# Performance work log

Hardware: AMD Instinct MI355X
Metric: run time of the kernel (lower is better)

The kernel has to match this reference:

```python
import jax, jax.numpy as jnp
import numpy as np
import math

C_IN, L, D, H, DFF = 16, 1024, 128, 8, 512
B = 16
EPS = 1e-5


def layer_norm(x, g, b):
    mu = jnp.mean(x, axis=-1, keepdims=True)
    var = jnp.var(x, axis=-1, keepdims=True)
    return (x - mu) * jax.lax.rsqrt(var + EPS) * g + b


def tape_pe():
    pos = jnp.arange(L, dtype=jnp.float32)[:, None]
    div = jnp.exp(jnp.arange(0, D, 2, dtype=jnp.float32) * (-math.log(10000.0) / D))
    ang = pos * div * (D / L)  # [L, D/2]
    return jnp.stack([jnp.sin(ang), jnp.cos(ang)], axis=-1).reshape(L, D)


def setup_inputs() -> dict:
    key = jax.random.key(0)
    ks = jax.random.split(key, 16)
    d4 = 4 * D
    inp = {
        "x": jax.random.normal(ks[0], (B, C_IN, L), dtype=jnp.float32),
        "conv1_w": jax.random.normal(ks[1], (d4, 1, 1, 7), dtype=jnp.float32) * 0.2,
        "conv1_b": jnp.zeros((d4,), jnp.float32),
        "bn1_g": jnp.ones((d4,), jnp.float32),
        "bn1_b": jnp.zeros((d4,), jnp.float32),
        "conv2_w": jax.random.normal(ks[2], (D, d4, C_IN, 1), dtype=jnp.float32) * (1.0 / math.sqrt(d4 * C_IN)),
        "conv2_b": jnp.zeros((D,), jnp.float32),
        "bn2_g": jnp.ones((D,), jnp.float32),
        "bn2_b": jnp.zeros((D,), jnp.float32),
        "wq": jax.random.normal(ks[3], (D, D), dtype=jnp.float32) / math.sqrt(D),
        "wk": jax.random.normal(ks[4], (D, D), dtype=jnp.float32) / math.sqrt(D),
        "wv": jax.random.normal(ks[5], (D, D), dtype=jnp.float32) / math.sqrt(D),
        "rel_table": jax.random.normal(ks[6], (2 * L - 1, H), dtype=jnp.float32) * 0.02,
        "ln_att_g": jnp.ones((D,), jnp.float32),
        "ln_att_b": jnp.zeros((D,), jnp.float32),
        "ln1_g": jnp.ones((D,), jnp.float32),
        "ln1_b": jnp.zeros((D,), jnp.float32),
        "ln2_g": jnp.ones((D,), jnp.float32),
        "ln2_b": jnp.zeros((D,), jnp.float32),
        "ff_w1": jax.random.normal(ks[7], (DFF, D), dtype=jnp.float32) / math.sqrt(D),
        "ff_b1": jnp.zeros((DFF,), jnp.float32),
        "ff_w2": jax.random.normal(ks[8], (D, DFF), dtype=jnp.float32) / math.sqrt(DFF),
        "ff_b2": jnp.zeros((D,), jnp.float32),
    }
    return inp


def reference(x, conv1_w, conv1_b, bn1_g, bn1_b, conv2_w, conv2_b, bn2_g, bn2_b,
              wq, wk, wv, rel_table, ln_att_g, ln_att_b, ln1_g, ln1_b,
              ln2_g, ln2_b, ff_w1, ff_b1, ff_w2, ff_b2):
    dn = ("NCHW", "OIHW", "NCHW")
    h = x[:, None, :, :]  # [B,1,C_IN,L]
    h = jax.lax.conv_general_dilated(h, conv1_w, (1, 1), ((0, 0), (3, 3)), dimension_numbers=dn)
    h = h + conv1_b[None, :, None, None]
    # BatchNorm2d in eval with running_mean=0, running_var=1
    h = h * (bn1_g * (1.0 / math.sqrt(1.0 + EPS)))[None, :, None, None] + bn1_b[None, :, None, None]
    h = jax.nn.gelu(h, approximate=False)
    h = jax.lax.conv_general_dilated(h, conv2_w, (1, 1), ((0, 0), (0, 0)), dimension_numbers=dn)
    h = h + conv2_b[None, :, None, None]
    h = h * (bn2_g * (1.0 / math.sqrt(1.0 + EPS)))[None, :, None, None] + bn2_b[None, :, None, None]
    h = jax.nn.gelu(h, approximate=False)
    x_src = jnp.transpose(h[:, :, 0, :], (0, 2, 1))  # [B,L,D]

    x_pos = x_src + tape_pe()  # tAPE (dropout is identity in eval)

    dh = D // H
    scale = D ** (-0.5)  # note: full d_model, as in the source
    q = (x_pos @ wq.T).reshape(B, L, H, dh).transpose(0, 2, 1, 3)
    k = (x_pos @ wk.T).reshape(B, L, H, dh).transpose(0, 2, 1, 3)
    v = (x_pos @ wv.T).reshape(B, L, H, dh).transpose(0, 2, 1, 3)
    scores = jnp.einsum("bhqd,bhkd->bhqk", q, k) * scale
    attn = jax.nn.softmax(scores, axis=-1)
    # gathered relative-position bias added AFTER softmax (faithful to source)
    idx = jnp.arange(L)[:, None] - jnp.arange(L)[None, :] + (L - 1)  # [L,L]
    rel_bias = rel_table[idx]  # [L,L,H]
    attn = attn + jnp.transpose(rel_bias, (2, 0, 1))[None]
    out = jnp.einsum("bhqk,bhkd->bhqd", attn, v).transpose(0, 2, 1, 3).reshape(B, L, D)
    out = layer_norm(out, ln_att_g, ln_att_b)  # Attention_Rel_Scl.to_out

    att = layer_norm(x_src + out, ln1_g, ln1_b)
    ff = jax.nn.relu(att @ ff_w1.T + ff_b1) @ ff_w2.T + ff_b2
    y = layer_norm(att + ff, ln2_g, ln2_b)
    return jnp.transpose(y, (0, 2, 1))  # [B,D,L]
```

## Files before the change

kernel.cpp:

```cpp
#include <hip/hip_runtime.h>
#include <math.h>

#define BB   16
#define CIN  16
#define LL   1024
#define DD   128
#define NHH  8
#define DHH  16
#define DF   512

#define INVS 0.9999950000374998f
#define QSCALE 0.08838834764831845f

typedef __attribute__((ext_vector_type(4))) float f32x4;
typedef __attribute__((ext_vector_type(8))) __bf16 bf16x8;

__device__ __forceinline__ float gelu_t(float v) {
    float u = v * v;
    float a = v * fmaf(-0.07135481627f, u, -1.5957691216f);
    float e = __expf(a);
    return v * __builtin_amdgcn_rcpf(1.0f + e);
}

__device__ __forceinline__ unsigned pkbf(float a, float b) {
    union { __bf16 h[2]; unsigned u; } z;
    z.h[0] = (__bf16)a; z.h[1] = (__bf16)b;
    return z.u;
}

#define SWZ(l) ((((l) & 7) ^ (((l) >> 2) & 6)))

__global__ __launch_bounds__(256) void k_prep(
    const float* __restrict__ c2w,
    const float* __restrict__ wq, const float* __restrict__ wk,
    const float* __restrict__ wv,
    const float* __restrict__ w1f, const float* __restrict__ w2f,
    const float* __restrict__ c1w, const float* __restrict__ c1b,
    const float* __restrict__ g1,  const float* __restrict__ bb1,
    __bf16* __restrict__ w2bf,  __bf16* __restrict__ wallbf,
    __bf16* __restrict__ w1fbf, __bf16* __restrict__ w2fbf,
    float* __restrict__ peb, float* __restrict__ w1A, float* __restrict__ b1A)
{
    const int bid = blockIdx.x;
    const int t = threadIdx.x;
    if (bid < 1024) {
        int i = (bid * 256 + t) * 4;
        float4 v = *(const float4*)&c2w[i];
        union { __bf16 h[4]; float2 f2; } u;
        u.h[0] = (__bf16)v.x; u.h[1] = (__bf16)v.y;
        u.h[2] = (__bf16)v.z; u.h[3] = (__bf16)v.w;
        *(float2*)&w2bf[i] = u.f2;
    } else if (bid < 1072) {
        int e = ((bid - 1024) * 256 + t) * 4;
        int sel = e >> 14, r = e & 16383;
        const float* src = (sel == 0) ? wq : ((sel == 1) ? wk : wv);
        float sc = (sel == 0) ? QSCALE : 1.0f;
        float4 v = *(const float4*)&src[r];
        union { __bf16 h[4]; float2 f2; } u;
        u.h[0] = (__bf16)(v.x * sc); u.h[1] = (__bf16)(v.y * sc);
        u.h[2] = (__bf16)(v.z * sc); u.h[3] = (__bf16)(v.w * sc);
        *(float2*)&wallbf[e] = u.f2;
    } else if (bid < 1136) {
        int e = ((bid - 1072) * 256 + t) * 4;
        float4 v = *(const float4*)&w1f[e];
        union { __bf16 h[4]; float2 f2; } u;
        u.h[0] = (__bf16)v.x; u.h[1] = (__bf16)v.y;
        u.h[2] = (__bf16)v.z; u.h[3] = (__bf16)v.w;
        *(float2*)&w1fbf[e] = u.f2;
    } else if (bid < 1200) {
        int e = ((bid - 1136) * 256 + t) * 4;
        float4 v = *(const float4*)&w2f[e];
        union { __bf16 h[4]; float2 f2; } u;
        u.h[0] = (__bf16)v.x; u.h[1] = (__bf16)v.y;
        u.h[2] = (__bf16)v.z; u.h[3] = (__bf16)v.w;
        *(float2*)&w2fbf[e] = u.f2;
    } else if (bid < 1456) {
        int p = (bid - 1200) * 256 + t;
        int l = p >> 6, jj = p & 63;
        float ang = (float)l * expf(-0.14391156831212787f * (float)jj) * 0.125f;
        peb[l * 128 + jj * 2]     = sinf(ang);
        peb[l * 128 + jj * 2 + 1] = cosf(ang);
    } else {
        for (int o = t; o < DF; o += 256) {
            float A = g1[o] * INVS;
            #pragma unroll
            for (int tp = 0; tp < 7; tp++) w1A[o * 8 + tp] = c1w[o * 7 + tp] * A;
            w1A[o * 8 + 7] = 0.0f;
            b1A[o] = fmaf(c1b[o], A, bb1[o]);
        }
    }
}

__global__ __launch_bounds__(256) void k_conv(
    const float* __restrict__ x,
    const float* __restrict__ w1A, const float* __restrict__ b1A,
    const __bf16* __restrict__ w2bf,
    const float* __restrict__ c2b, const float* __restrict__ g2,
    const float* __restrict__ bb2,
    float* __restrict__ xsrc)
{
    const int lt = blockIdx.x;
    const int b  = blockIdx.y;
    const int t  = threadIdx.x;
    const int l0 = lt * 32;

    __shared__ float xs[CIN][40];
    __shared__ __align__(16) __bf16 Ab[2][32 * 128];

    for (int idx = t; idx < CIN * 38; idx += 256) {
        int c = idx / 38, i = idx % 38;
        int l = l0 - 3 + i;
        xs[c][i] = (l >= 0 && l < LL) ? x[(b * CIN + c) * LL + l] : 0.0f;
    }
    __syncthreads();

    const int cp  = t & 7;
    const int lqi = (t >> 3) & 7;
    const int ogu = __builtin_amdgcn_readfirstlane(t >> 6);
    const int c0  = cp * 2;
    const int lq  = lqi * 4;

    float xw[2][10];
    #pragma unroll
    for (int j = 0; j < 10; j++) {
        xw[0][j] = xs[c0][lq + j];
        xw[1][j] = xs[c0 + 1][lq + j];
    }

    const int lane = t & 63;
    const int l15 = lane & 15, kg = lane >> 4;
    const int nw = t >> 6;

    f32x4 acc[2][2];
    #pragma unroll
    for (int mf = 0; mf < 2; mf++)
        #pragma unroll
        for (int nf = 0; nf < 2; nf++) acc[mf][nf] = (f32x4){0.f, 0.f, 0.f, 0.f};

    bf16x8 breg[2][8];

#define BLOAD(CH, BUF) do { \
    _Pragma("unroll") \
    for (int nf = 0; nf < 2; nf++) \
        _Pragma("unroll") \
        for (int kk = 0; kk < 4; kk++) \
            breg[BUF][nf * 4 + kk] = *(const bf16x8*)&w2bf[ \
                (size_t)(nw * 32 + nf * 16 + l15) * 8192 + (size_t)(CH) * 128 + kk * 32 + kg * 8]; \
} while (0)

#define CONV_CHUNK(BUF, CH) do { \
    _Pragma("unroll") \
    for (int j = 0; j < 2; j++) { \
        int o = (CH) * 8 + ogu * 2 + j; \
        f32x4 wA = *(const f32x4*)&w1A[o * 8]; \
        f32x4 wB = *(const f32x4*)&w1A[o * 8 + 4]; \
        float bias = b1A[o]; \
        int kcol = (ogu * 2 + j) * 16 + c0; \
        _Pragma("unroll") \
        for (int dl = 0; dl < 4; dl++) { \
            float h2[2]; \
            _Pragma("unroll") \
            for (int ci = 0; ci < 2; ci++) { \
                float s = fmaf(xw[ci][dl], wA[0], bias); \
                s = fmaf(xw[ci][dl + 1], wA[1], s); \
                s = fmaf(xw[ci][dl + 2], wA[2], s); \
                s = fmaf(xw[ci][dl + 3], wA[3], s); \
                s = fmaf(xw[ci][dl + 4], wB[0], s); \
                s = fmaf(xw[ci][dl + 5], wB[1], s); \
                s = fmaf(xw[ci][dl + 6], wB[2], s); \
                h2[ci] = gelu_t(s); \
            } \
            int l = lq + dl; \
            *(unsigned*)&Ab[BUF][l * 128 + (kcol ^ (SWZ(l) << 3))] = pkbf(h2[0], h2[1]); \
        } \
    } \
} while (0)

#define MFMA_CHUNK(BUF, BI) do { \
    _Pragma("unroll") \
    for (int kk = 0; kk < 4; kk++) { \
        int kb = kk * 32 + kg * 8; \
        bf16x8 af[2]; \
        _Pragma("unroll") \
        for (int mf = 0; mf < 2; mf++) { \
            int r = mf * 16 + l15; \
            af[mf] = *(const bf16x8*)&Ab[BUF][r * 128 + (kb ^ (SWZ(r) << 3))]; \
        } \
        _Pragma("unroll") \
        for (int mf = 0; mf < 2; mf++) \
            _Pragma("unroll") \
            for (int nf = 0; nf < 2; nf++) \
                acc[mf][nf] = __builtin_amdgcn_mfma_f32_16x16x32_bf16( \
                    af[mf], breg[BI][nf * 4 + kk], acc[mf][nf], 0, 0, 0); \
    } \
} while (0)

    BLOAD(0, 0);
    CONV_CHUNK(0, 0);
    __syncthreads();

    for (int ic = 0; ic < 62; ic += 2) {
        BLOAD(ic + 1, 1);
        MFMA_CHUNK(0, 0);
        CONV_CHUNK(1, ic + 1);
        __syncthreads();

        BLOAD(ic + 2, 0);
        MFMA_CHUNK(1, 1);
        CONV_CHUNK(0, ic + 2);
        __syncthreads();
    }
    BLOAD(63, 1);
    MFMA_CHUNK(0, 0);
    CONV_CHUNK(1, 63);
    __syncthreads();
    MFMA_CHUNK(1, 1);

    #pragma unroll
    for (int mf = 0; mf < 2; mf++) {
        #pragma unroll
        for (int nf = 0; nf < 2; nf++) {
            int d = nw * 32 + nf * 16 + l15;
            float A2 = g2[d] * INVS;
            float B2 = fmaf(c2b[d], A2, bb2[d]);
            #pragma unroll
            for (int r = 0; r < 4; r++) {
                int l = l0 + mf * 16 + kg * 4 + r;
                xsrc[((size_t)b * LL + l) * DD + d] = gelu_t(fmaf(acc[mf][nf][r], A2, B2));
            }
        }
    }
#undef BLOAD
#undef CONV_CHUNK
#undef MFMA_CHUNK
}

__global__ __launch_bounds__(384) void k_qkv(
    const float* __restrict__ xsrc, const float* __restrict__ peb,
    const __bf16* __restrict__ wallbf,
    __bf16* __restrict__ qo, __bf16* __restrict__ ko, __bf16* __restrict__ vo)
{
    const int lt = blockIdx.x, b = blockIdx.y;
    const int t = threadIdx.x;
    const int l0 = lt * 64;

    __shared__ __align__(16) __bf16 Xp[64 * 128];

    for (int e = t; e < 2048; e += 384) {
        int l = e >> 5, d0 = (e & 31) * 4;
        float4 xv = *(const float4*)&xsrc[((size_t)b * LL + l0 + l) * DD + d0];
        float4 pv = *(const float4*)&peb[(size_t)(l0 + l) * DD + d0];
        union { __bf16 h[4]; float2 f2; } u;
        u.h[0] = (__bf16)(xv.x + pv.x); u.h[1] = (__bf16)(xv.y + pv.y);
        u.h[2] = (__bf16)(xv.z + pv.z); u.h[3] = (__bf16)(xv.w + pv.w);
        *(float2*)&Xp[l * 128 + (d0 ^ (SWZ(l) << 3))] = u.f2;
    }
    __syncthreads();

    const int w = t >> 6, lane = t & 63;
    const int l15 = lane & 15, kg = lane >> 4;
    const int wsel = w >> 1, hb = w & 1;

    bf16x8 breg[16];
    #pragma unroll
    for (int nf = 0; nf < 4; nf++)
        #pragma unroll
        for (int kk = 0; kk < 4; kk++)
            breg[nf * 4 + kk] = *(const bf16x8*)&wallbf[
                (size_t)wsel * 16384 + (size_t)(hb * 64 + nf * 16 + l15) * 128 + kk * 32 + kg * 8];

    f32x4 acc[4][4];
    #pragma unroll
    for (int mf = 0; mf < 4; mf++)
        #pragma unroll
        for (int nf = 0; nf < 4; nf++) acc[mf][nf] = (f32x4){0.f, 0.f, 0.f, 0.f};

    #pragma unroll
    for (int kk = 0; kk < 4; kk++) {
        int kb = kk * 32 + kg * 8;
        bf16x8 af[4];
        #pragma unroll
        for (int mf = 0; mf < 4; mf++) {
            int r = mf * 16 + l15;
            af[mf] = *(const bf16x8*)&Xp[r * 128 + (kb ^ (SWZ(r) << 3))];
        }
        #pragma unroll
        for (int mf = 0; mf < 4; mf++)
            #pragma unroll
            for (int nf = 0; nf < 4; nf++)
                acc[mf][nf] = __builtin_amdgcn_mfma_f32_16x16x32_bf16(
                    af[mf], breg[nf * 4 + kk], acc[mf][nf], 0, 0, 0);
    }

    __bf16* op = (wsel == 0) ? qo : ((wsel == 1) ? ko : vo);
    #pragma unroll
    for (int mf = 0; mf < 4; mf++) {
        #pragma unroll
        for (int nf = 0; nf < 4; nf++) {
            int h = hb * 4 + nf;
            #pragma unroll
            for (int r = 0; r < 4; r++) {
                int l = l0 + mf * 16 + kg * 4 + r;
                op[(((size_t)b * NHH + h) * LL + l) * DHH + l15] = (__bf16)acc[mf][nf][r];
            }
        }
    }
}

__global__ __launch_bounds__(256) void k_attn(
    const __bf16* __restrict__ q, const __bf16* __restrict__ k,
    const __bf16* __restrict__ v, const float* __restrict__ rel,
    float* __restrict__ out)
{
    const int bh = blockIdx.x;
    const int qt = blockIdx.y;
    const int h  = bh & 7;
    const int t  = threadIdx.x;
    const int w  = t >> 6, lane = t & 63;
    const int g  = lane >> 4, qi = lane & 15;
    const int xq = (qi & 7) << 3;
    const int qbase = qt * 128 + w * 32;

    __shared__ __align__(16) __bf16 lds[16384];
    __bf16* Vl = lds;
    __bf16* Pw = lds + 4096 + w * 2048;
    __bf16* R0 = lds + 12288;
    __bf16* R1 = lds + 14336;

    for (int i = t; i < 2048; i += 256) {
        R0[i] = (__bf16)((i <= 2046) ? rel[(size_t)(2046 - i) * NHH + h] : 0.0f);
        R1[i] = (__bf16)((i <= 2045) ? rel[(size_t)(2045 - i) * NHH + h] : 0.0f);
    }

    bf16x8 qf[2];
    {
        union { unsigned u[4]; bf16x8 v8; } uz;
        uz.u[0] = uz.u[1] = uz.u[2] = uz.u[3] = 0u;
        #pragma unroll
        for (int n = 0; n < 2; n++) {
            qf[n] = uz.v8;
            if (g < 2)
                qf[n] = *(const bf16x8*)&q[((size_t)bh * LL + qbase + n * 16 + qi) * DHH + g * 8];
        }
    }

    f32x4 accp[2], accb[2];
    #pragma unroll
    for (int n = 0; n < 2; n++) {
        accp[n] = (f32x4){0.f, 0.f, 0.f, 0.f};
        accb[n] = (f32x4){0.f, 0.f, 0.f, 0.f};
    }
    float mrun[2] = {-INFINITY, -INFINITY};
    float lrun[2] = {0.f, 0.f};

    const f32x4 zero4 = (f32x4){0.f, 0.f, 0.f, 0.f};

#define PROC_N(Sn, n) do { \
    float mx = Sn[0][0]; \
    _Pragma("unroll") \
    for (int f = 0; f < 8; f++) { \
        _Pragma("unroll") \
        for (int r = 0; r < 4; r++) if (f || r) mx = fmaxf(mx, Sn[f][r]); } \
    mx = fmaxf(mx, __shfl_xor(mx, 16, 64)); \
    mx = fmaxf(mx, __shfl_xor(mx, 32, 64)); \
    float mnew = fmaxf(mrun[n], mx); \
    float sf = __expf(mrun[n] - mnew); \
    mrun[n] = mnew; \
    lrun[n] *= sf; \
    accp[n][0] *= sf; accp[n][1] *= sf; accp[n][2] *= sf; accp[n][3] *= sf; \
    float ls = 0.f; \
    _Pragma("unroll") \
    for (int f = 0; f < 8; f++) { \
        float p0 = __expf(Sn[f][0] - mnew), p1 = __expf(Sn[f][1] - mnew); \
        float p2 = __expf(Sn[f][2] - mnew), p3 = __expf(Sn[f][3] - mnew); \
        ls += (p0 + p1) + (p2 + p3); \
        unsigned* pp = (unsigned*)(Pw + (qi * 128 + ((f * 16 + g * 4) ^ xq))); \
        pp[0] = pkbf(p0, p1); pp[1] = pkbf(p2, p3); \
    } \
    ls += __shfl_xor(ls, 16, 64); ls += __shfl_xor(ls, 32, 64); \
    lrun[n] += ls; \
    int qoff = 1023 - (qbase + (n) * 16 + qi) + k0; \
    _Pragma("unroll") \
    for (int c = 0; c < 4; c++) { \
        bf16x8 vf = *(const bf16x8*)&Vbuf[qi * 128 + ((c * 32 + g * 8) ^ xq)]; \
        bf16x8 pf = *(const bf16x8*)&Pw[qi * 128 + ((c * 32 + g * 8) ^ xq)]; \
        int idx = qoff + c * 32 + 8 * g; \
        const unsigned* tb = (const unsigned*)((idx & 1) ? R1 : R0); \
        unsigned s_ = (unsigned)idx >> 1; \
        union { unsigned u[4]; bf16x8 v8; } bu; \
        bu.u[0] = tb[s_]; bu.u[1] = tb[s_ + 1]; \
        bu.u[2] = tb[s_ + 2]; bu.u[3] = tb[s_ + 3]; \
        accp[n] = __builtin_amdgcn_mfma_f32_16x16x32_bf16(vf, pf, accp[n], 0, 0, 0); \
        accb[n] = __builtin_amdgcn_mfma_f32_16x16x32_bf16(vf, bu.v8, accb[n], 0, 0, 0); \
    } \
} while (0)

    for (int kt = 0; kt < 8; kt++) {
        const int k0 = kt * 128;
        {
            int kr = t >> 1, d0 = (t & 1) * 8;
            bf16x8 b8 = *(const bf16x8*)&v[((size_t)bh * LL + k0 + kr) * DHH + d0];
            __bf16* dst = Vl + (kt & 1) * 2048;
            #pragma unroll
            for (int i = 0; i < 8; i++) {
                int d = d0 + i;
                dst[d * 128 + (kr ^ ((d & 7) << 3))] = b8[i];
            }
        }
        __syncthreads();
        const __bf16* Vbuf = Vl + (kt & 1) * 2048;

        f32x4 S0[8], S1[8];
        #pragma unroll
        for (int f = 0; f < 8; f++) {
            bf16x8 kf = *(const bf16x8*)&k[((size_t)bh * LL + k0 + f * 16 + qi) * DHH + (g & 1) * 8];
            S0[f] = __builtin_amdgcn_mfma_f32_16x16x32_bf16(kf, qf[0], zero4, 0, 0, 0);
            S1[f] = __builtin_amdgcn_mfma_f32_16x16x32_bf16(kf, qf[1], zero4, 0, 0, 0);
        }

        PROC_N(S0, 0);
        PROC_N(S1, 1);
    }
#undef PROC_N

    #pragma unroll
    for (int n = 0; n < 2; n++) {
        float inv = 1.0f / lrun[n];
        float4 o;
        o.x = accp[n][0] * inv + accb[n][0];
        o.y = accp[n][1] * inv + accb[n][1];
        o.z = accp[n][2] * inv + accb[n][2];
        o.w = accp[n][3] * inv + accb[n][3];
        *(float4*)&out[((size_t)bh * LL + qbase + n * 16 + qi) * DHH + g * 4] = o;
    }
}

__global__ __launch_bounds__(256) void k_ln(
    const float* __restrict__ ao,  const float* __restrict__ xsrc,
    const float* __restrict__ lag, const float* __restrict__ lab,
    const float* __restrict__ l1g, const float* __restrict__ l1b,
    float* __restrict__ att)
{
    const int lt = blockIdx.x, b = blockIdx.y;
    const int t = threadIdx.x;
    const int l0 = lt * 64;
    __shared__ float tile[64][132];

    #pragma unroll
    for (int u = 0; u < 4; u++) {
        int cid = u * 256 + t;
        int hh = cid >> 7, rem = cid & 127;
        int l = rem >> 1, dh0 = (rem & 1) * 8;
        const float* src = &ao[(((size_t)b * NHH + hh) * LL + l0 + l) * DHH + dh0];
        float4 a0 = *(const float4*)src;
        float4 a1 = *(const float4*)(src + 4);
        *(float4*)&tile[l][hh * 16 + dh0]     = a0;
        *(float4*)&tile[l][hh * 16 + dh0 + 4] = a1;
    }
    __syncthreads();

    const int wid = t >> 6, lane = t & 63;
    float2 ga  = *(const float2*)&lag[lane * 2];
    float2 ba  = *(const float2*)&lab[lane * 2];
    float2 g1v = *(const float2*)&l1g[lane * 2];
    float2 b1v = *(const float2*)&l1b[lane * 2];

    for (int rr = 0; rr < 16; rr++) {
        int r = wid * 16 + rr;
        float2 vv = *(const float2*)&tile[r][lane * 2];
        float s = vv.x + vv.y, s2 = vv.x * vv.x + vv.y * vv.y;
        #pragma unroll
        for (int m = 1; m < 64; m <<= 1) { s += __shfl_xor(s, m, 64); s2 += __shfl_xor(s2, m, 64); }
        float mu = s * (1.f / 128.f);
        float var = s2 * (1.f / 128.f) - mu * mu;
        float rs = rsqrtf(var + 1e-5f);
        float o0 = (vv.x - mu) * rs * ga.x + ba.x;
        float o1 = (vv.y - mu) * rs * ga.y + ba.y;
        float2 xv = *(const float2*)&xsrc[((size_t)b * LL + l0 + r) * DD + lane * 2];
        float t0 = xv.x + o0, t1 = xv.y + o1;
        s = t0 + t1; s2 = t0 * t0 + t1 * t1;
        #pragma unroll
        for (int m = 1; m < 64; m <<= 1) { s += __shfl_xor(s, m, 64); s2 += __shfl_xor(s2, m, 64); }
        mu = s * (1.f / 128.f);
        var = s2 * (1.f / 128.f) - mu * mu;
        rs = rsqrtf(var + 1e-5f);
        float a0 = (t0 - mu) * rs * g1v.x + b1v.x;
        float a1 = (t1 - mu) * rs * g1v.y + b1v.y;
        float2 o = {a0, a1};
        *(float2*)&att[((size_t)b * LL + l0 + r) * DD + lane * 2] = o;
    }
}

__global__ __launch_bounds__(512) void k_ff1(
    const float* __restrict__ att, const __bf16* __restrict__ w1fbf,
    const float* __restrict__ b1f, __bf16* __restrict__ ff1b)
{
    const int lt = blockIdx.x, b = blockIdx.y;
    const int t = threadIdx.x;
    const int l0 = lt * 64;

    __shared__ __align__(16) __bf16 Ax[64 * 128];

    #pragma unroll
    for (int it = 0; it < 4; it++) {
        int e = it * 512 + t;
        int l = e >> 5, d0 = (e & 31) * 4;
        float4 xv = *(const float4*)&att[((size_t)b * LL + l0 + l) * DD + d0];
        union { __bf16 h[4]; float2 f2; } u;
        u.h[0] = (__bf16)xv.x; u.h[1] = (__bf16)xv.y;
        u.h[2] = (__bf16)xv.z; u.h[3] = (__bf16)xv.w;
        *(float2*)&Ax[l * 128 + (d0 ^ (SWZ(l) << 3))] = u.f2;
    }
    __syncthreads();

    const int w = t >> 6, lane = t & 63;
    const int l15 = lane & 15, kg = lane >> 4;

    bf16x8 breg[16];
    #pragma unroll
    for (int nf = 0; nf < 4; nf++)
        #pragma unroll
        for (int kk = 0; kk < 4; kk++)
            breg[nf * 4 + kk] = *(const bf16x8*)&w1fbf[
                (size_t)(w * 64 + nf * 16 + l15) * 128 + kk * 32 + kg * 8];

    f32x4 acc[4][4];
    #pragma unroll
    for (int mf = 0; mf < 4; mf++)
        #pragma unroll
        for (int nf = 0; nf < 4; nf++) acc[mf][nf] = (f32x4){0.f, 0.f, 0.f, 0.f};

    #pragma unroll
    for (int kk = 0; kk < 4; kk++) {
        int kb = kk * 32 + kg * 8;
        bf16x8 af[4];
        #pragma unroll
        for (int mf = 0; mf < 4; mf++) {
            int r = mf * 16 + l15;
            af[mf] = *(const bf16x8*)&Ax[r * 128 + (kb ^ (SWZ(r) << 3))];
        }
        #pragma unroll
        for (int mf = 0; mf < 4; mf++)
            #pragma unroll
            for (int nf = 0; nf < 4; nf++)
                acc[mf][nf] = __builtin_amdgcn_mfma_f32_16x16x32_bf16(
                    af[mf], breg[nf * 4 + kk], acc[mf][nf], 0, 0, 0);
    }

    #pragma unroll
    for (int nf = 0; nf < 4; nf++) {
        int n = w * 64 + nf * 16 + l15;
        float bias = b1f[n];
        #pragma unroll
        for (int mf = 0; mf < 4; mf++) {
            #pragma unroll
            for (int r = 0; r < 4; r++) {
                int l = l0 + mf * 16 + kg * 4 + r;
                float vv = fmaxf(acc[mf][nf][r] + bias, 0.0f);
                ff1b[((size_t)b * LL + l) * DF + n] = (__bf16)vv;
            }
        }
    }
}

__global__ __launch_bounds__(512) void k_ff2(
    const __bf16* __restrict__ ff1b, const __bf16* __restrict__ w2fbf,
    const float* __restrict__ b2f, const float* __restrict__ att,
    const float* __restrict__ l2g, const float* __restrict__ l2b,
    float* __restrict__ y)
{
    const int lt = blockIdx.x, b = blockIdx.y;
    const int t = threadIdx.x;
    const int l0 = lt * 64;

    __shared__ __align__(16) __bf16 Ax[64 * 512];
    float* yl = (float*)Ax;

    #pragma unroll
    for (int it = 0; it < 8; it++) {
        int g8 = it * 512 + t;
        int l = g8 >> 6, c8 = g8 & 63;
        bf16x8 v8 = *(const bf16x8*)&ff1b[((size_t)b * LL + l0 + l) * DF + c8 * 8];
        *(bf16x8*)&Ax[l * 512 + ((c8 * 8) ^ (SWZ(l) << 3))] = v8;
    }
    __syncthreads();

    const int w = t >> 6, lane = t & 63;
    const int l15 = lane & 15, kg = lane >> 4;
    const int d = w * 16 + l15;

    bf16x8 breg[16];
    #pragma unroll
    for (int kk = 0; kk < 16; kk++)
        breg[kk] = *(const bf16x8*)&w2fbf[(size_t)d * DF + kk * 32 + kg * 8];

    f32x4 acc[4];
    #pragma unroll
    for (int mf = 0; mf < 4; mf++) acc[mf] = (f32x4){0.f, 0.f, 0.f, 0.f};

    #pragma unroll
    for (int kk = 0; kk < 16; kk++) {
        int kb = kk * 32 + kg * 8;
        #pragma unroll
        for (int mf = 0; mf < 4; mf++) {
            int r = mf * 16 + l15;
            bf16x8 af = *(const bf16x8*)&Ax[r * 512 + (kb ^ (SWZ(r) << 3))];
            acc[mf] = __builtin_amdgcn_mfma_f32_16x16x32_bf16(af, breg[kk], acc[mf], 0, 0, 0);
        }
    }
    __syncthreads();

    {
        float bias = b2f[d];
        #pragma unroll
        for (int mf = 0; mf < 4; mf++) {
            #pragma unroll
            for (int r = 0; r < 4; r++) {
                int l = mf * 16 + kg * 4 + r;
                float res = att[((size_t)b * LL + l0 + l) * DD + d];
                yl[l * 132 + d] = acc[mf][r] + bias + res;
            }
        }
    }
    __syncthreads();

    const int wid = t >> 6;
    float2 gv = *(const float2*)&l2g[lane * 2];
    float2 bv = *(const float2*)&l2b[lane * 2];
    for (int rr = 0; rr < 8; rr++) {
        int r = wid * 8 + rr;
        float2 vv = *(const float2*)&yl[r * 132 + lane * 2];
        float s = vv.x + vv.y, s2 = vv.x * vv.x + vv.y * vv.y;
        #pragma unroll
        for (int m = 1; m < 64; m <<= 1) { s += __shfl_xor(s, m, 64); s2 += __shfl_xor(s2, m, 64); }
        float mu = s * (1.f / 128.f);
        float var = s2 * (1.f / 128.f) - mu * mu;
        float rs = rsqrtf(var + 1e-5f);
        float o0 = (vv.x - mu) * rs * gv.x + bv.x;
        float o1 = (vv.y - mu) * rs * gv.y + bv.y;
        yl[r * 132 + lane * 2]     = o0;
        yl[r * 132 + lane * 2 + 1] = o1;
    }
    __syncthreads();

    {
        int dd = t >> 2, lh = (t & 3) * 16;
        #pragma unroll
        for (int i0 = 0; i0 < 16; i0 += 4) {
            float4 o = { yl[(lh + i0 + 0) * 132 + dd], yl[(lh + i0 + 1) * 132 + dd],
                         yl[(lh + i0 + 2) * 132 + dd], yl[(lh + i0 + 3) * 132 + dd] };
            *(float4*)&y[(size_t)b * DD * LL + (size_t)dd * LL + l0 + lh + i0] = o;
        }
    }
}

extern "C" void kernel_launch(void* const* d_in, const int* in_sizes, int n_in,
                              void* d_out, int out_size, void* d_ws, size_t ws_size,
                              hipStream_t stream)
{
    const float* x   = (const float*)d_in[0];
    const float* c1w = (const float*)d_in[1];
    const float* c1b = (const float*)d_in[2];
    const float* g1  = (const float*)d_in[3];
    const float* bb1 = (const float*)d_in[4];
    const float* c2w = (const float*)d_in[5];
    const float* c2b = (const float*)d_in[6];
    const float* g2  = (const float*)d_in[7];
    const float* bb2 = (const float*)d_in[8];
    const float* wq  = (const float*)d_in[9];
    const float* wk  = (const float*)d_in[10];
    const float* wv  = (const float*)d_in[11];
    const float* rel = (const float*)d_in[12];
    const float* lag = (const float*)d_in[13];
    const float* lab = (const float*)d_in[14];
    const float* l1g = (const float*)d_in[15];
    const float* l1b = (const float*)d_in[16];
    const float* l2g = (const float*)d_in[17];
    const float* l2b = (const float*)d_in[18];
    const float* w1f = (const float*)d_in[19];
    const float* b1f = (const float*)d_in[20];
    const float* w2f = (const float*)d_in[21];
    const float* b2f = (const float*)d_in[22];

    char* W = (char*)d_ws;
    const size_t MB = 1ull << 20;
    float*  xsrc   = (float*)(W);
    float*  abuf   = (float*)(W + 8 * MB);
    float*  attb   = (float*)(W + 16 * MB);
    __bf16* qbuf   = (__bf16*)(W + 24 * MB);
    __bf16* kbuf   = (__bf16*)(W + 28 * MB);
    __bf16* vbuf   = (__bf16*)(W + 32 * MB);
    __bf16* ff1b   = (__bf16*)(W + 36 * MB);
    __bf16* w2bf   = (__bf16*)(W + 52 * MB);
    __bf16* wallbf = (__bf16*)(W + 54 * MB);
    __bf16* w1fbf  = (__bf16*)(W + 54 * MB + 128 * 1024);
    __bf16* w2fbf  = (__bf16*)(W + 54 * MB + 256 * 1024);
    float*  peb    = (float*)(W + 54 * MB + 384 * 1024);
    float*  w1A    = (float*)(W + 54 * MB + 896 * 1024);
    float*  b1A    = (float*)(W + 54 * MB + 912 * 1024);

    k_prep<<<dim3(1457), dim3(256), 0, stream>>>(
        c2w, wq, wk, wv, w1f, w2f, c1w, c1b, g1, bb1,
        w2bf, wallbf, w1fbf, w2fbf, peb, w1A, b1A);
    k_conv<<<dim3(32, 16), dim3(256), 0, stream>>>(x, w1A, b1A, w2bf, c2b, g2, bb2, xsrc);
    k_qkv<<<dim3(16, 16), dim3(384), 0, stream>>>(xsrc, peb, wallbf, qbuf, kbuf, vbuf);
    k_attn<<<dim3(128, 8), dim3(256), 0, stream>>>(qbuf, kbuf, vbuf, rel, abuf);
    k_ln<<<dim3(16, 16), dim3(256), 0, stream>>>(abuf, xsrc, lag, lab, l1g, l1b, attb);
    k_ff1<<<dim3(16, 16), dim3(512), 0, stream>>>(attb, w1fbf, b1f, ff1b);
    k_ff2<<<dim3(16, 16), dim3(512), 0, stream>>>(ff1b, w2fbf, b2f, attb, l2g, l2b, (float*)d_out);
}
```

Measured before the change: 246.4 us.

## Use 512-thread conv blocks with 256-wide K chunks and one N-fragment per wave

The fused conv kernel moves from 4 to 8 waves per block. Each wave now owns one 16-column output fragment instead of two, and each K chunk doubles to 256, giving 32 iterations instead of 64. This halves the number of block barriers and spreads the GELU conv generation over more threads, which should raise occupancy and latency hiding. In exchange the B-operand double-buffering in registers is dropped, so weight loads are issued after each MFMA chunk rather than overlapped one chunk ahead, and LDS use per block doubles.

```diff
diff --git a/kernel.cpp b/kernel.cpp
--- a/kernel.cpp
+++ b/kernel.cpp
@@ -91,7 +91,7 @@
     }
 }
 
-__global__ __launch_bounds__(256) void k_conv(
+__global__ __launch_bounds__(512, 4) void k_conv(
     const float* __restrict__ x,
     const float* __restrict__ w1A, const float* __restrict__ b1A,
     const __bf16* __restrict__ w2bf,
@@ -105,20 +105,22 @@
     const int l0 = lt * 32;
 
     __shared__ float xs[CIN][40];
-    __shared__ __align__(16) __bf16 Ab[2][32 * 128];
-
-    for (int idx = t; idx < CIN * 38; idx += 256) {
+    __shared__ __align__(16) __bf16 Ab[2][32 * 256];
+
+    for (int idx = t; idx < CIN * 38; idx += 512) {
         int c = idx / 38, i = idx % 38;
         int l = l0 - 3 + i;
         xs[c][i] = (l >= 0 && l < LL) ? x[(b * CIN + c) * LL + l] : 0.0f;
     }
     __syncthreads();
 
-    const int cp  = t & 7;
-    const int lqi = (t >> 3) & 7;
-    const int ogu = __builtin_amdgcn_readfirstlane(t >> 6);
-    const int c0  = cp * 2;
-    const int lq  = lqi * 4;
+    const int lane = t & 63;
+    const int wv   = t >> 6;
+    const int ogu  = __builtin_amdgcn_readfirstlane(wv);
+    const int cp   = lane & 7;
+    const int lqi  = lane >> 3;
+    const int c0   = cp * 2;
+    const int lq   = lqi * 4;
 
     float xw[2][10];
     #pragma unroll
@@ -127,31 +129,25 @@
         xw[1][j] = xs[c0 + 1][lq + j];
     }
 
-    const int lane = t & 63;
     const int l15 = lane & 15, kg = lane >> 4;
-    const int nw = t >> 6;
-
-    f32x4 acc[2][2];
-    #pragma unroll
-    for (int mf = 0; mf < 2; mf++)
-        #pragma unroll
-        for (int nf = 0; nf < 2; nf++) acc[mf][nf] = (f32x4){0.f, 0.f, 0.f, 0.f};
-
-    bf16x8 breg[2][8];
-
-#define BLOAD(CH, BUF) do { \
+
+    f32x4 acc[2];
+    acc[0] = (f32x4){0.f, 0.f, 0.f, 0.f};
+    acc[1] = (f32x4){0.f, 0.f, 0.f, 0.f};
+
+    bf16x8 breg[8];
+
+#define BLOAD(CH) do { \
     _Pragma("unroll") \
-    for (int nf = 0; nf < 2; nf++) \
-        _Pragma("unroll") \
-        for (int kk = 0; kk < 4; kk++) \
-            breg[BUF][nf * 4 + kk] = *(const bf16x8*)&w2bf[ \
-                (size_t)(nw * 32 + nf * 16 + l15) * 8192 + (size_t)(CH) * 128 + kk * 32 + kg * 8]; \
+    for (int kk = 0; kk < 8; kk++) \
+        breg[kk] = *(const bf16x8*)&w2bf[ \
+            (size_t)(wv * 16 + l15) * 8192 + (size_t)(CH) * 256 + kk * 32 + kg * 8]; \
 } while (0)
 
 #define CONV_CHUNK(BUF, CH) do { \
     _Pragma("unroll") \
     for (int j = 0; j < 2; j++) { \
-        int o = (CH) * 8 + ogu * 2 + j; \
+        int o = (CH) * 16 + ogu * 2 + j; \
         f32x4 wA = *(const f32x4*)&w1A[o * 8]; \
         f32x4 wB = *(const f32x4*)&w1A[o * 8 + 4]; \
         float bias = b1A[o]; \
@@ -171,62 +167,55 @@
                 h2[ci] = gelu_t(s); \
             } \
             int l = lq + dl; \
-            *(unsigned*)&Ab[BUF][l * 128 + (kcol ^ (SWZ(l) << 3))] = pkbf(h2[0], h2[1]); \
+            *(unsigned*)&Ab[BUF][l * 256 + (kcol ^ (SWZ(l) << 3))] = pkbf(h2[0], h2[1]); \
         } \
     } \
 } while (0)
 
-#define MFMA_CHUNK(BUF, BI) do { \
+#define MFMA_CHUNK(BUF) do { \
     _Pragma("unroll") \
-    for (int kk = 0; kk < 4; kk++) { \
+    for (int kk = 0; kk < 8; kk++) { \
         int kb = kk * 32 + kg * 8; \
-        bf16x8 af[2]; \
         _Pragma("unroll") \
         for (int mf = 0; mf < 2; mf++) { \
             int r = mf * 16 + l15; \
-            af[mf] = *(const bf16x8*)&Ab[BUF][r * 128 + (kb ^ (SWZ(r) << 3))]; \
+            bf16x8 af = *(const bf16x8*)&Ab[BUF][r * 256 + (kb ^ (SWZ(r) << 3))]; \
+            acc[mf] = __builtin_amdgcn_mfma_f32_16x16x32_bf16(af, breg[kk], acc[mf], 0, 0, 0); \
         } \
-        _Pragma("unroll") \
-        for (int mf = 0; mf < 2; mf++) \
-            _Pragma("unroll") \
-            for (int nf = 0; nf < 2; nf++) \
-                acc[mf][nf] = __builtin_amdgcn_mfma_f32_16x16x32_bf16( \
-                    af[mf], breg[BI][nf * 4 + kk], acc[mf][nf], 0, 0, 0); \
     } \
 } while (0)
 
-    BLOAD(0, 0);
+    BLOAD(0);
     CONV_CHUNK(0, 0);
     __syncthreads();
 
-    for (int ic = 0; ic < 62; ic += 2) {
-        BLOAD(ic + 1, 1);
-        MFMA_CHUNK(0, 0);
+    for (int ic = 0; ic < 30; ic += 2) {
+        MFMA_CHUNK(0);
+        BLOAD(ic + 1);
         CONV_CHUNK(1, ic + 1);
         __syncthreads();
 
-        BLOAD(ic + 2, 0);
-        MFMA_CHUNK(1, 1);
+        MFMA_CHUNK(1);
+        BLOAD(ic + 2);
         CONV_CHUNK(0, ic + 2);
         __syncthreads();
     }
-    BLOAD(63, 1);
-    MFMA_CHUNK(0, 0);
-    CONV_CHUNK(1, 63);
-    __syncthreads();
-    MFMA_CHUNK(1, 1);
-
-    #pragma unroll
-    for (int mf = 0; mf < 2; mf++) {
-        #pragma unroll
-        for (int nf = 0; nf < 2; nf++) {
-            int d = nw * 32 + nf * 16 + l15;
-            float A2 = g2[d] * INVS;
-            float B2 = fmaf(c2b[d], A2, bb2[d]);
+    MFMA_CHUNK(0);
+    BLOAD(31);
+    CONV_CHUNK(1, 31);
+    __syncthreads();
+    MFMA_CHUNK(1);
+
+    {
+        int d = wv * 16 + l15;
+        float A2 = g2[d] * INVS;
+        float B2 = fmaf(c2b[d], A2, bb2[d]);
+        #pragma unroll
+        for (int mf = 0; mf < 2; mf++) {
             #pragma unroll
             for (int r = 0; r < 4; r++) {
                 int l = l0 + mf * 16 + kg * 4 + r;
-                xsrc[((size_t)b * LL + l) * DD + d] = gelu_t(fmaf(acc[mf][nf][r], A2, B2));
+                xsrc[((size_t)b * LL + l) * DD + d] = gelu_t(fmaf(acc[mf][r], A2, B2));
             }
         }
     }
@@ -702,7 +691,7 @@
     k_prep<<<dim3(1457), dim3(256), 0, stream>>>(
         c2w, wq, wk, wv, w1f, w2f, c1w, c1b, g1, bb1,
         w2bf, wallbf, w1fbf, w2fbf, peb, w1A, b1A);
-    k_conv<<<dim3(32, 16), dim3(256), 0, stream>>>(x, w1A, b1A, w2bf, c2b, g2, bb2, xsrc);
+    k_conv<<<dim3(32, 16), dim3(512), 0, stream>>>(x, w1A, b1A, w2bf, c2b, g2, bb2, xsrc);
     k_qkv<<<dim3(16, 16), dim3(384), 0, stream>>>(xsrc, peb, wallbf, qbuf, kbuf, vbuf);
     k_attn<<<dim3(128, 8), dim3(256), 0, stream>>>(qbuf, kbuf, vbuf, rel, abuf);
     k_ln<<<dim3(16, 16), dim3(256), 0, stream>>>(abuf, xsrc, lag, lab, l1g, l1b, attb);
```

After: 240.7 us. 2.3% less time.
